# Kernel tuning notes

Hardware: AMD Instinct MI355X
Metric: run time of the kernel (lower is better)

The kernel has to match this reference:

```python
import jax, jax.numpy as jnp
import numpy as np

N_BATCH = 50000
N_FEATURE = 128
DEPTH = 9
N_TREE = 200
N_NODE = 2 ** (DEPTH + 1) - 1  # complete binary tree, 1023 nodes
N_OUTPUT = 8
TREE_LEAF = -1


def setup_inputs() -> dict:
    key = jax.random.key(0)
    kx, kf, kt, kv = jax.random.split(key, 4)
    x = jax.random.normal(kx, (N_BATCH, N_FEATURE), dtype=jnp.float32)

    n_internal = 2 ** DEPTH - 1
    idx = np.arange(N_NODE)
    internal = idx < n_internal
    cl = np.where(internal, 2 * idx + 1, TREE_LEAF).astype(np.int32)
    cr = np.where(internal, 2 * idx + 2, TREE_LEAF).astype(np.int32)
    children_left = jnp.tile(jnp.asarray(cl)[None, :], (N_TREE, 1))
    children_right = jnp.tile(jnp.asarray(cr)[None, :], (N_TREE, 1))

    # random split features at internal nodes, -2 (undefined) at leaves
    feat_rand = jax.random.randint(kf, (N_TREE, N_NODE), 0, N_FEATURE, dtype=jnp.int32)
    feature = jnp.where(jnp.asarray(internal)[None, :], feat_rand, jnp.int32(-2))

    threshold = jax.random.normal(kt, (N_TREE, N_NODE), dtype=jnp.float32)
    value = jax.random.normal(kv, (N_TREE, N_NODE, N_OUTPUT), dtype=jnp.float32)

    return {
        "x": x,
        "feature": feature,
        "threshold": threshold,
        "children_left": children_left,
        "children_right": children_right,
        "value": value,
    }


def reference(x, feature, threshold, children_left, children_right, value):
    n_batch = x.shape[0]
    n_tree = feature.shape[0]
    tidx = jnp.arange(n_tree)[None, :]  # [1, T] broadcasts against node [B, T]

    # pad x with a zero column; leaf nodes (feature < 0) index this column
    xp = jnp.pad(x, ((0, 0), (0, 1)))  # [B, F+1]

    node = jnp.zeros((n_batch, n_tree), dtype=jnp.int32)  # start at root
    for _ in range(DEPTH):
        feat = feature[tidx, node]                       # [B, T]
        feat = jnp.where(feat < 0, N_FEATURE, feat)
        xval = jnp.take_along_axis(xp, feat, axis=1)     # [B, T]
        split = threshold[tidx, node]                    # [B, T]
        lchild = children_left[tidx, node]               # [B, T]
        rchild = children_right[tidx, node]              # [B, T]
        new_node = jnp.where(xval <= split, lchild, rchild)
        # stay put once a leaf marker (-1) is produced
        node = jnp.where(new_node > TREE_LEAF, new_node, node)

    val = value[tidx, node]          # [B, T, n_output]
    out = jnp.mean(val, axis=1)      # activation: mean over trees -> [B, n_output]
    return out
```

## Files before the change

### kernel.cpp

```cpp
#include <hip/hip_runtime.h>

#define N_BATCH   50000
#define N_FEATURE 128
#define DEPTH     9
#define N_TREE    200
#define N_NODE    1023
#define N_OUTPUT  8

#define BPB     64
#define BLOCK   256
#define TPR     8
#define ROUNDS  (N_TREE / TPR)

#define FULL_CHUNKS 768
#define NCHUNK      ((N_BATCH + BPB - 1) / BPB)
#define TAIL_CHUNKS (NCHUNK - FULL_CHUNKS)
#define TAIL_SPLIT  ROUNDS
#define TAIL_BLOCKS (TAIL_CHUNKS * TAIL_SPLIT)
#define GRID        (FULL_CHUNKS + TAIL_BLOCKS)

#define TREE_B  2560
#define WAVE_B  (2 * TREE_B)
#define REC_B   (4 * WAVE_B)

__global__ __launch_bounds__(BLOCK, 3)
void tree_kernel(const float* __restrict__ x,
                 const int*   __restrict__ feature,
                 const float* __restrict__ threshold,
                 const float* __restrict__ value,
                 float*       __restrict__ out)
{
    __shared__ float xt[N_FEATURE * BPB];
    __shared__ __align__(16) char recbuf[REC_B];

    const int tid = threadIdx.x;
    const int bid = blockIdx.x;
    const int b   = tid & 63;
    const int g   = tid >> 6;
    char* wbuf = recbuf + g * WAVE_B;

    int chunk, r0, r1; bool tail;
    if (bid < FULL_CHUNKS) { chunk = bid; r0 = 0; r1 = ROUNDS; tail = false; }
    else {
        const int t2 = bid - FULL_CHUNKS;
        chunk = FULL_CHUNKS + t2 / TAIL_SPLIT;
        r0 = t2 % TAIL_SPLIT; r1 = r0 + 1; tail = true;
    }

    float thr[2][8]; int fr[2][8];
    #pragma unroll
    for (int u = 0; u < 2; ++u) {
        const int base = (r0 * TPR + 2 * g + u) * N_NODE;
        #pragma unroll
        for (int j = 0; j < 8; ++j) {
            const int s = b + j * 64;
            thr[u][j] = threshold[base + s];
            fr[u][j]  = feature[base + s];
        }
    }

    {
        const float4* x4 = (const float4*)x;
        float4* R = (float4*)recbuf;
        #pragma unroll
        for (int rr = 0; rr < 2; ++rr) {
            #pragma unroll
            for (int k = 0; k < 4; ++k) {
                const int j  = tid + k * BLOCK;
                const int bl = j >> 5, f4 = j & 31;
                const int gb = chunk * BPB + rr * 32 + bl;
                float4 v = (gb < N_BATCH) ? x4[(size_t)gb * 32 + f4]
                                          : make_float4(0.f, 0.f, 0.f, 0.f);
                R[bl * 32 + (f4 ^ bl)] = v;
            }
            __syncthreads();
            {
                const int b32 = tid & 31, fc = tid >> 5;
                const int bb = rr * 32 + b32;
                #pragma unroll
                for (int c = 0; c < 4; ++c) {
                    const int f4 = fc * 4 + c;
                    float4 v = R[b32 * 32 + (f4 ^ b32)];
                    xt[(f4 * 4 + 0) * BPB + bb] = v.x;
                    xt[(f4 * 4 + 1) * BPB + bb] = v.y;
                    xt[(f4 * 4 + 2) * BPB + bb] = v.z;
                    xt[(f4 * 4 + 3) * BPB + bb] = v.w;
                }
            }
            __syncthreads();
        }
    }

    float acc[N_OUTPUT];
    #pragma unroll
    for (int o = 0; o < N_OUTPUT; ++o) acc[o] = 0.f;

    float*          tb0f = (float*)wbuf;
    unsigned char*  fb0  = (unsigned char*)(wbuf + 2048);
    float*          tb1f = (float*)(wbuf + TREE_B);
    unsigned char*  fb1  = (unsigned char*)(wbuf + TREE_B + 2048);

    for (int r = r0; r < r1; ++r) {
        __asm__ volatile("s_waitcnt lgkmcnt(0)" ::: "memory");
        #pragma unroll
        for (int u = 0; u < 2; ++u) {
            char* tb = wbuf + u * TREE_B;
            #pragma unroll
            for (int j = 0; j < 8; ++j) {
                const int s   = b + j * 64;
                const int dst = (s == 0) ? 511 : s - 1;
                ((float*)tb)[dst] = thr[u][j];
                ((unsigned char*)(tb + 2048))[dst] = (unsigned char)fr[u][j];
            }
        }
        __asm__ volatile("s_waitcnt lgkmcnt(0)" ::: "memory");

        if (r + 1 < r1) {
            #pragma unroll
            for (int u = 0; u < 2; ++u) {
                const int base = ((r + 1) * TPR + 2 * g + u) * N_NODE;
                #pragma unroll
                for (int j = 0; j < 8; ++j) {
                    const int s = b + j * 64;
                    thr[u][j] = threshold[base + s];
                    fr[u][j]  = feature[base + s];
                }
            }
        }

        int n0 = 0, n1 = 0;
        float th0 = tb0f[511], th1 = tb1f[511];
        int   fv0 = fb0[511],  fv1 = fb1[511];
        float2 c0 = ((float2*)tb0f)[0], c1 = ((float2*)tb1f)[0];
        int   k0 = ((unsigned short*)fb0)[0], k1 = ((unsigned short*)fb1)[0];
        #pragma unroll
        for (int d = 0; d < DEPTH; ++d) {
            const float xv0 = xt[fv0 * BPB + b];
            const float xv1 = xt[fv1 * BPB + b];
            const int s0 = (xv0 > th0) ? 1 : 0;
            const int s1 = (xv1 > th1) ? 1 : 0;
            n0 = 2 * n0 + 1 + s0;
            n1 = 2 * n1 + 1 + s1;
            if (d < DEPTH - 1) {
                th0 = s0 ? c0.y : c0.x;  fv0 = (k0 >> (s0 << 3)) & 255;
                th1 = s1 ? c1.y : c1.x;  fv1 = (k1 >> (s1 << 3)) & 255;
            }
            if (d < DEPTH - 2) {
                c0 = ((float2*)tb0f)[n0]; k0 = ((unsigned short*)fb0)[n0];
                c1 = ((float2*)tb1f)[n1]; k1 = ((unsigned short*)fb1)[n1];
            }
        }
        {
            const int gt0 = r * TPR + 2 * g;
            const float4* v0 = (const float4*)(value + ((size_t)gt0 * N_NODE + n0) * N_OUTPUT);
            const float4* v1 = (const float4*)(value + ((size_t)(gt0 + 1) * N_NODE + n1) * N_OUTPUT);
            const float4 a0 = v0[0], a1 = v0[1];
            const float4 d0 = v1[0], d1 = v1[1];
            acc[0] += a0.x + d0.x;  acc[1] += a0.y + d0.y;
            acc[2] += a0.z + d0.z;  acc[3] += a0.w + d0.w;
            acc[4] += a1.x + d1.x;  acc[5] += a1.y + d1.y;
            acc[6] += a1.z + d1.z;  acc[7] += a1.w + d1.w;
        }
    }

    __syncthreads();
    float* red = (float*)recbuf;
    {
        float* dst = red + (g * 576 + b * 9);
        #pragma unroll
        for (int o = 0; o < N_OUTPUT; ++o) dst[o] = acc[o];
    }
    __syncthreads();
    {
        const int bl = tid >> 2, o0 = (tid & 3) * 2;
        const int bg = chunk * BPB + bl;
        if (bg < N_BATCH) {
            float s0 = 0.f, s1 = 0.f;
            #pragma unroll
            for (int gg = 0; gg < 4; ++gg) {
                s0 += red[gg * 576 + bl * 9 + o0];
                s1 += red[gg * 576 + bl * 9 + o0 + 1];
            }
            if (!tail) {
                float2 res;
                res.x = s0 * (1.0f / N_TREE);
                res.y = s1 * (1.0f / N_TREE);
                ((float2*)out)[(size_t)chunk * 256 + tid] = res;
            } else {
                atomicAdd(out + (size_t)bg * N_OUTPUT + o0,     s0 * (1.0f / N_TREE));
                atomicAdd(out + (size_t)bg * N_OUTPUT + o0 + 1, s1 * (1.0f / N_TREE));
            }
        }
    }
}

extern "C" void kernel_launch(void* const* d_in, const int* in_sizes, int n_in,
                              void* d_out, int out_size, void* d_ws, size_t ws_size,
                              hipStream_t stream) {
    const float* x         = (const float*)d_in[0];
    const int*   feature   = (const int*)d_in[1];
    const float* threshold = (const float*)d_in[2];
    const float* value     = (const float*)d_in[5];
    float* out = (float*)d_out;

    const size_t tail_off = (size_t)FULL_CHUNKS * BPB * N_OUTPUT;
    if ((size_t)out_size > tail_off) {
        hipMemsetAsync(out + tail_off, 0, ((size_t)out_size - tail_off) * sizeof(float), stream);
    }

    tree_kernel<<<dim3(GRID), dim3(BLOCK), 0, stream>>>(x, feature, threshold, value, out);
}
```

Before: 138.7 us.

## Use 8 waves per block with one tree per wave instead of two

The block grows from 4 to 8 waves, and each wave now traverses a single tree per round instead of two interleaved trees. Per-wave LDS tree storage halves, and the x staging and final reduction are adjusted for 512 threads. The launch bound now requests 6 blocks per CU. This raises thread-level parallelism and lowers per-thread register pressure, but it drops the per-thread ILP of two independent traversal chains and doubles the reduction width.

Result: faster. 135.2 us (-2.5%).

```diff
diff --git a/kernel.cpp b/kernel.cpp
--- a/kernel.cpp
+++ b/kernel.cpp
@@ -8,7 +8,8 @@
 #define N_OUTPUT  8
 
 #define BPB     64
-#define BLOCK   256
+#define WAVES   8
+#define BLOCK   (WAVES * 64)
 #define TPR     8
 #define ROUNDS  (N_TREE / TPR)
 
@@ -20,10 +21,9 @@
 #define GRID        (FULL_CHUNKS + TAIL_BLOCKS)
 
 #define TREE_B  2560
-#define WAVE_B  (2 * TREE_B)
-#define REC_B   (4 * WAVE_B)
+#define REC_B   (WAVES * TREE_B)
 
-__global__ __launch_bounds__(BLOCK, 3)
+__global__ __launch_bounds__(BLOCK, 6)
 void tree_kernel(const float* __restrict__ x,
                  const int*   __restrict__ feature,
                  const float* __restrict__ threshold,
@@ -37,7 +37,7 @@
     const int bid = blockIdx.x;
     const int b   = tid & 63;
     const int g   = tid >> 6;
-    char* wbuf = recbuf + g * WAVE_B;
+    char* wbuf = recbuf + g * TREE_B;
 
     int chunk, r0, r1; bool tail;
     if (bid < FULL_CHUNKS) { chunk = bid; r0 = 0; r1 = ROUNDS; tail = false; }
@@ -47,17 +47,13 @@
         r0 = t2 % TAIL_SPLIT; r1 = r0 + 1; tail = true;
     }
 
-    float thr[2][8]; int fr[2][8];
+    const float* tpre = threshold + (size_t)(r0 * TPR + g) * N_NODE + b;
+    const int*   fpre = feature   + (size_t)(r0 * TPR + g) * N_NODE + b;
+    const float* vbase = value + (size_t)(r0 * TPR + g) * N_NODE * N_OUTPUT;
+
+    float thr[8]; int fr[8];
     #pragma unroll
-    for (int u = 0; u < 2; ++u) {
-        const int base = (r0 * TPR + 2 * g + u) * N_NODE;
-        #pragma unroll
-        for (int j = 0; j < 8; ++j) {
-            const int s = b + j * 64;
-            thr[u][j] = threshold[base + s];
-            fr[u][j]  = feature[base + s];
-        }
-    }
+    for (int j = 0; j < 8; ++j) { thr[j] = tpre[j * 64]; fr[j] = fpre[j * 64]; }
 
     {
         const float4* x4 = (const float4*)x;
@@ -65,7 +61,7 @@
         #pragma unroll
         for (int rr = 0; rr < 2; ++rr) {
             #pragma unroll
-            for (int k = 0; k < 4; ++k) {
+            for (int k = 0; k < 2; ++k) {
                 const int j  = tid + k * BLOCK;
                 const int bl = j >> 5, f4 = j & 31;
                 const int gb = chunk * BPB + rr * 32 + bl;
@@ -78,8 +74,8 @@
                 const int b32 = tid & 31, fc = tid >> 5;
                 const int bb = rr * 32 + b32;
                 #pragma unroll
-                for (int c = 0; c < 4; ++c) {
-                    const int f4 = fc * 4 + c;
+                for (int c = 0; c < 2; ++c) {
+                    const int f4 = fc * 2 + c;
                     float4 v = R[b32 * 32 + (f4 ^ b32)];
                     xt[(f4 * 4 + 0) * BPB + bb] = v.x;
                     xt[(f4 * 4 + 1) * BPB + bb] = v.y;
@@ -95,72 +91,53 @@
     #pragma unroll
     for (int o = 0; o < N_OUTPUT; ++o) acc[o] = 0.f;
 
-    float*          tb0f = (float*)wbuf;
-    unsigned char*  fb0  = (unsigned char*)(wbuf + 2048);
-    float*          tb1f = (float*)(wbuf + TREE_B);
-    unsigned char*  fb1  = (unsigned char*)(wbuf + TREE_B + 2048);
+    float*         thS = (float*)wbuf;
+    unsigned char* fS  = (unsigned char*)(wbuf + 2048);
 
     for (int r = r0; r < r1; ++r) {
         __asm__ volatile("s_waitcnt lgkmcnt(0)" ::: "memory");
         #pragma unroll
-        for (int u = 0; u < 2; ++u) {
-            char* tb = wbuf + u * TREE_B;
-            #pragma unroll
-            for (int j = 0; j < 8; ++j) {
-                const int s   = b + j * 64;
-                const int dst = (s == 0) ? 511 : s - 1;
-                ((float*)tb)[dst] = thr[u][j];
-                ((unsigned char*)(tb + 2048))[dst] = (unsigned char)fr[u][j];
-            }
+        for (int j = 0; j < 8; ++j) {
+            const int dst = (b + j * 64 - 1) & 511;
+            thS[dst] = thr[j];
+            fS[dst]  = (unsigned char)fr[j];
         }
         __asm__ volatile("s_waitcnt lgkmcnt(0)" ::: "memory");
 
         if (r + 1 < r1) {
+            const float* tn = tpre + TPR * N_NODE;
+            const int*   fn = fpre + TPR * N_NODE;
             #pragma unroll
-            for (int u = 0; u < 2; ++u) {
-                const int base = ((r + 1) * TPR + 2 * g + u) * N_NODE;
-                #pragma unroll
-                for (int j = 0; j < 8; ++j) {
-                    const int s = b + j * 64;
-                    thr[u][j] = threshold[base + s];
-                    fr[u][j]  = feature[base + s];
-                }
-            }
+            for (int j = 0; j < 8; ++j) { thr[j] = tn[j * 64]; fr[j] = fn[j * 64]; }
+            tpre = tn; fpre = fn;
         }
 
-        int n0 = 0, n1 = 0;
-        float th0 = tb0f[511], th1 = tb1f[511];
-        int   fv0 = fb0[511],  fv1 = fb1[511];
-        float2 c0 = ((float2*)tb0f)[0], c1 = ((float2*)tb1f)[0];
-        int   k0 = ((unsigned short*)fb0)[0], k1 = ((unsigned short*)fb1)[0];
+        int n = 0;
+        float th = thS[511];
+        int   fv = fS[511];
+        float2 c = ((float2*)thS)[0];
+        int   k  = ((unsigned short*)fS)[0];
         #pragma unroll
         for (int d = 0; d < DEPTH; ++d) {
-            const float xv0 = xt[fv0 * BPB + b];
-            const float xv1 = xt[fv1 * BPB + b];
-            const int s0 = (xv0 > th0) ? 1 : 0;
-            const int s1 = (xv1 > th1) ? 1 : 0;
-            n0 = 2 * n0 + 1 + s0;
-            n1 = 2 * n1 + 1 + s1;
+            const float xv = xt[fv * BPB + b];
+            const int s = (xv > th) ? 1 : 0;
+            n = 2 * n + 1 + s;
             if (d < DEPTH - 1) {
-                th0 = s0 ? c0.y : c0.x;  fv0 = (k0 >> (s0 << 3)) & 255;
-                th1 = s1 ? c1.y : c1.x;  fv1 = (k1 >> (s1 << 3)) & 255;
+                th = s ? c.y : c.x;
+                fv = (k >> (s << 3)) & 255;
             }
             if (d < DEPTH - 2) {
-                c0 = ((float2*)tb0f)[n0]; k0 = ((unsigned short*)fb0)[n0];
-                c1 = ((float2*)tb1f)[n1]; k1 = ((unsigned short*)fb1)[n1];
+                c = ((float2*)thS)[n];
+                k = ((unsigned short*)fS)[n];
             }
         }
         {
-            const int gt0 = r * TPR + 2 * g;
-            const float4* v0 = (const float4*)(value + ((size_t)gt0 * N_NODE + n0) * N_OUTPUT);
-            const float4* v1 = (const float4*)(value + ((size_t)(gt0 + 1) * N_NODE + n1) * N_OUTPUT);
-            const float4 a0 = v0[0], a1 = v0[1];
-            const float4 d0 = v1[0], d1 = v1[1];
-            acc[0] += a0.x + d0.x;  acc[1] += a0.y + d0.y;
-            acc[2] += a0.z + d0.z;  acc[3] += a0.w + d0.w;
-            acc[4] += a1.x + d1.x;  acc[5] += a1.y + d1.y;
-            acc[6] += a1.z + d1.z;  acc[7] += a1.w + d1.w;
+            const float4* vp = (const float4*)(vbase + (size_t)n * N_OUTPUT);
+            const float4 a0 = vp[0], a1 = vp[1];
+            acc[0] += a0.x; acc[1] += a0.y; acc[2] += a0.z; acc[3] += a0.w;
+            acc[4] += a1.x; acc[5] += a1.y; acc[6] += a1.z; acc[7] += a1.w;
         }
+        vbase += (size_t)TPR * N_NODE * N_OUTPUT;
     }
 
     __syncthreads();
@@ -172,24 +149,16 @@
     }
     __syncthreads();
     {
-        const int bl = tid >> 2, o0 = (tid & 3) * 2;
+        const int bl = tid >> 3, o = tid & 7;
         const int bg = chunk * BPB + bl;
-        if (bg < N_BATCH) {
-            float s0 = 0.f, s1 = 0.f;
-            #pragma unroll
-            for (int gg = 0; gg < 4; ++gg) {
-                s0 += red[gg * 576 + bl * 9 + o0];
-                s1 += red[gg * 576 + bl * 9 + o0 + 1];
-            }
-            if (!tail) {
-                float2 res;
-                res.x = s0 * (1.0f / N_TREE);
-                res.y = s1 * (1.0f / N_TREE);
-                ((float2*)out)[(size_t)chunk * 256 + tid] = res;
-            } else {
-                atomicAdd(out + (size_t)bg * N_OUTPUT + o0,     s0 * (1.0f / N_TREE));
-                atomicAdd(out + (size_t)bg * N_OUTPUT + o0 + 1, s1 * (1.0f / N_TREE));
-            }
+        float s = 0.f;
+        #pragma unroll
+        for (int gg = 0; gg < WAVES; ++gg) s += red[gg * 576 + bl * 9 + o];
+        s *= (1.0f / N_TREE);
+        if (!tail) {
+            out[(size_t)chunk * (BPB * N_OUTPUT) + tid] = s;
+        } else if (bg < N_BATCH) {
+            atomicAdd(out + (size_t)bg * N_OUTPUT + o, s);
         }
     }
 }
```
